# Kernel tuning notes

Measured on AMD Instinct MI355X. Metric: run time of the kernel, lower is better.

## Reference

```python
import jax, jax.numpy as jnp
import numpy as np

NEG_INF_DIAG = 1000000.0

def setup_inputs() -> dict:
    key = jax.random.key(0)
    k1, k2, k3 = jax.random.split(key, 3)
    B, N, S, D = 64, 32, 256, 128
    return {
        "query_embeddings": jax.random.normal(k1, (B, N, D), dtype=jnp.float32),
        "doc_embeddings": jax.random.normal(k2, (B, S, D), dtype=jnp.float32),
        "neg_doc_embeddings": jax.random.normal(k3, (B, S, D), dtype=jnp.float32),
    }

def _maxsim(q, d):
    # q: (b, n, dim), d: (b, s, dim) -> (b,) sum over n of max over s of q.d
    return jnp.einsum('bnd,bsd->bns', q, d).max(axis=2).sum(axis=1)

def reference(query_embeddings, doc_embeddings, neg_doc_embeddings):
    pos_scores = _maxsim(query_embeddings, doc_embeddings)
    neg_scores = _maxsim(query_embeddings, neg_doc_embeddings)
    loss = jax.nn.softplus(neg_scores - pos_scores).mean()

    # in-batch term: scores[b, c] = MaxSim(query b, doc c)
    scores = jnp.einsum('bnd,csd->bcns', query_embeddings, doc_embeddings).max(axis=3).sum(axis=2)  # (B, B)
    pos = jnp.diagonal(scores)
    B = scores.shape[0]
    neg = (scores - jnp.eye(B, dtype=scores.dtype) * NEG_INF_DIAG).max(axis=1)
    loss = loss + jax.nn.softplus(neg - pos).mean()
    return loss / 2
```

## Files before the change

kernel.cpp:

```cpp
#include <hip/hip_runtime.h>
#include <hip/hip_bf16.h>

#define B_SZ 64

typedef __attribute__((ext_vector_type(8))) short bf16x8;
typedef __attribute__((ext_vector_type(4))) float f32x4;

static __device__ __forceinline__ unsigned short f2bf(float f) {
    __hip_bfloat16 h = __float2bfloat16(f);
    return *reinterpret_cast<unsigned short*>(&h);
}

static __device__ __forceinline__ bf16x8 cvt_frag(const float* __restrict__ src) {
    float4 a = reinterpret_cast<const float4*>(src)[0];
    float4 b = reinterpret_cast<const float4*>(src)[1];
    union { bf16x8 v; unsigned short u[8]; } t;
    t.u[0] = f2bf(a.x); t.u[1] = f2bf(a.y); t.u[2] = f2bf(a.z); t.u[3] = f2bf(a.w);
    t.u[4] = f2bf(b.x); t.u[5] = f2bf(b.y); t.u[6] = f2bf(b.z); t.u[7] = f2bf(b.w);
    return t.v;
}

#define MFMA(A, Bv, C) __builtin_amdgcn_mfma_f32_16x16x32_bf16(A, Bv, C, 0, 0, 0)

__global__ __launch_bounds__(256, 2) void maxsim_mega(const float* __restrict__ q,
                                                      const float* __restrict__ dd,
                                                      const float* __restrict__ nd,
                                                      float* __restrict__ scores) {
    const int wg  = blockIdx.x;
    const int tid = threadIdx.x;
    const int wave = tid >> 6, lane = tid & 63;
    const int l15 = lane & 15, lhi = lane >> 4;

    __shared__ bf16x8 docL[4096];
    __shared__ bf16x8 qL[512];
    __shared__ float wred[8][4][4][8];

    int c, b0, nb;
    const float* docp;
    if (wg < 512) {
        const int x = wg & 7, i = wg >> 3;
        c   = x * 8 + (i & 7);
        b0  = (i >> 3) * 8;
        nb  = 8;
        docp = dd + (size_t)c * 32768;
    } else {
        b0 = wg - 512; c = 64; nb = 1;
        docp = nd + (size_t)b0 * 32768;
    }

    char* lb = reinterpret_cast<char*>(docL);
    #pragma unroll
    for (int i = 0; i < 16; ++i) {
        const int rem_g = i * 256 + tid;
        bf16x8 v = cvt_frag(docp + (size_t)rem_g * 8);
        const int ch = rem_g >> 10, rem = rem_g & 1023;
        const int a = ch * 16384 + ((rem * 16) ^ (((rem >> 4) & 7) << 4));
        *reinterpret_cast<bf16x8*>(lb + a) = v;
    }
    __syncthreads();

    bf16x8 Bv[4][4];
    #pragma unroll
    for (int kk = 0; kk < 4; ++kk)
        #pragma unroll
        for (int nt = 0; nt < 4; ++nt) {
            const int rem = (nt * 16 + l15) * 16 + kk * 4 + lhi;
            const int a = wave * 16384 + ((rem * 16) ^ (((rem >> 4) & 7) << 4));
            Bv[kk][nt] = *reinterpret_cast<const bf16x8*>(lb + a);
        }

    for (int bi = 0; bi < nb; ++bi) {
        const int b = b0 + bi;
        #pragma unroll
        for (int h = 0; h < 2; ++h) {
            const int g  = h * 256 + tid;
            const int n  = ((g >> 6) & 1) * 16 + (g & 15);
            const int k8 = (g >> 7) * 4 + ((g >> 4) & 3);
            qL[g] = cvt_frag(q + (size_t)b * 4096 + (size_t)(n * 16 + k8) * 8);
        }
        __syncthreads();

        bf16x8 Af[4][2];
        #pragma unroll
        for (int kk = 0; kk < 4; ++kk) {
            Af[kk][0] = qL[kk * 128 + lane];
            Af[kk][1] = qL[kk * 128 + 64 + lane];
        }
        f32x4 acc[2][4] = {};
        #pragma unroll
        for (int kk = 0; kk < 4; ++kk)
            #pragma unroll
            for (int nt = 0; nt < 4; ++nt) {
                acc[0][nt] = MFMA(Af[kk][0], Bv[kk][nt], acc[0][nt]);
                acc[1][nt] = MFMA(Af[kk][1], Bv[kk][nt], acc[1][nt]);
            }
        #pragma unroll
        for (int mt = 0; mt < 2; ++mt)
            #pragma unroll
            for (int r = 0; r < 4; ++r) {
                float m = fmaxf(fmaxf(acc[mt][0][r], acc[mt][1][r]),
                                fmaxf(acc[mt][2][r], acc[mt][3][r]));
                m = fmaxf(m, __shfl_xor(m, 1, 64));
                m = fmaxf(m, __shfl_xor(m, 2, 64));
                m = fmaxf(m, __shfl_xor(m, 4, 64));
                m = fmaxf(m, __shfl_xor(m, 8, 64));
                if (l15 == 0) wred[bi][wave][lhi][mt * 4 + r] = m;
            }
        __syncthreads();
    }

    if (tid < nb * 32) {
        const int bi = tid >> 5, n = tid & 31;
        const int slot = (n >> 4) * 4 + (n & 3);
        const int lh   = (n >> 2) & 3;
        float m = fmaxf(fmaxf(wred[bi][0][lh][slot], wred[bi][1][lh][slot]),
                        fmaxf(wred[bi][2][lh][slot], wred[bi][3][lh][slot]));
        m += __shfl_xor(m, 1, 32);
        m += __shfl_xor(m, 2, 32);
        m += __shfl_xor(m, 4, 32);
        m += __shfl_xor(m, 8, 32);
        m += __shfl_xor(m, 16, 32);
        if (n == 0) scores[(size_t)(b0 + bi) * 65 + c] = m;
    }
}

static __device__ __forceinline__ float softplusf(float x) {
    return fmaxf(x, 0.0f) + log1pf(expf(-fabsf(x)));
}

__global__ __launch_bounds__(64) void loss_kernel(const float* __restrict__ scores,
                                                  float* __restrict__ out) {
    const int b = threadIdx.x;
    const float* row = scores + b * 65;
    const float pos  = row[b];
    const float negq = row[64];
    float nib = -1e30f;
    #pragma unroll
    for (int c = 0; c < B_SZ; ++c) {
        float v = row[c] - ((c == b) ? 1000000.0f : 0.0f);
        nib = fmaxf(nib, v);
    }
    float t = softplusf(negq - pos) + softplusf(nib - pos);
    t += __shfl_xor(t, 1, 64);
    t += __shfl_xor(t, 2, 64);
    t += __shfl_xor(t, 4, 64);
    t += __shfl_xor(t, 8, 64);
    t += __shfl_xor(t, 16, 64);
    t += __shfl_xor(t, 32, 64);
    if (b == 0) out[0] = t * (0.5f / 64.0f);
}

extern "C" void kernel_launch(void* const* d_in, const int* in_sizes, int n_in,
                              void* d_out, int out_size, void* d_ws, size_t ws_size,
                              hipStream_t stream) {
    const float* q  = (const float*)d_in[0];
    const float* dd = (const float*)d_in[1];
    const float* nd = (const float*)d_in[2];
    float* out = (float*)d_out;

    float* scores = (float*)d_ws;

    maxsim_mega<<<512 + B_SZ, 256, 0, stream>>>(q, dd, nd, scores);
    loss_kernel<<<1, 64, 0, stream>>>(scores, out);
}
```

Before: 96.73 us.

## Load MFMA fragments directly from global memory, dropping LDS staging

Result: slower. 119.5 us (+23.6%).

```diff
diff --git a/kernel.cpp b/kernel.cpp
--- a/kernel.cpp
+++ b/kernel.cpp
@@ -22,17 +22,15 @@
 
 #define MFMA(A, Bv, C) __builtin_amdgcn_mfma_f32_16x16x32_bf16(A, Bv, C, 0, 0, 0)
 
-__global__ __launch_bounds__(256, 2) void maxsim_mega(const float* __restrict__ q,
-                                                      const float* __restrict__ dd,
-                                                      const float* __restrict__ nd,
-                                                      float* __restrict__ scores) {
+__global__ __launch_bounds__(256, 3) void maxsim_direct(const float* __restrict__ q,
+                                                        const float* __restrict__ dd,
+                                                        const float* __restrict__ nd,
+                                                        float* __restrict__ scores) {
     const int wg  = blockIdx.x;
     const int tid = threadIdx.x;
     const int wave = tid >> 6, lane = tid & 63;
     const int l15 = lane & 15, lhi = lane >> 4;
 
-    __shared__ bf16x8 docL[4096];
-    __shared__ bf16x8 qL[512];
     __shared__ float wred[8][4][4][8];
 
     int c, b0, nb;
@@ -48,43 +46,24 @@
         docp = nd + (size_t)b0 * 32768;
     }
 
-    char* lb = reinterpret_cast<char*>(docL);
-    #pragma unroll
-    for (int i = 0; i < 16; ++i) {
-        const int rem_g = i * 256 + tid;
-        bf16x8 v = cvt_frag(docp + (size_t)rem_g * 8);
-        const int ch = rem_g >> 10, rem = rem_g & 1023;
-        const int a = ch * 16384 + ((rem * 16) ^ (((rem >> 4) & 7) << 4));
-        *reinterpret_cast<bf16x8*>(lb + a) = v;
+    bf16x8 Bv[4][4];
+    {
+        const float* base = docp + (size_t)(wave * 64 + l15) * 128 + lhi * 8;
+        #pragma unroll
+        for (int kk = 0; kk < 4; ++kk)
+            #pragma unroll
+            for (int nt = 0; nt < 4; ++nt)
+                Bv[kk][nt] = cvt_frag(base + nt * 16 * 128 + kk * 32);
     }
-    __syncthreads();
 
-    bf16x8 Bv[4][4];
-    #pragma unroll
-    for (int kk = 0; kk < 4; ++kk)
-        #pragma unroll
-        for (int nt = 0; nt < 4; ++nt) {
-            const int rem = (nt * 16 + l15) * 16 + kk * 4 + lhi;
-            const int a = wave * 16384 + ((rem * 16) ^ (((rem >> 4) & 7) << 4));
-            Bv[kk][nt] = *reinterpret_cast<const bf16x8*>(lb + a);
-        }
-
+    const float* qbase = q + (size_t)b0 * 4096 + (size_t)l15 * 128 + lhi * 8;
     for (int bi = 0; bi < nb; ++bi) {
-        const int b = b0 + bi;
-        #pragma unroll
-        for (int h = 0; h < 2; ++h) {
-            const int g  = h * 256 + tid;
-            const int n  = ((g >> 6) & 1) * 16 + (g & 15);
-            const int k8 = (g >> 7) * 4 + ((g >> 4) & 3);
-            qL[g] = cvt_frag(q + (size_t)b * 4096 + (size_t)(n * 16 + k8) * 8);
-        }
-        __syncthreads();
-
         bf16x8 Af[4][2];
+        const float* qb = qbase + (size_t)bi * 4096;
         #pragma unroll
         for (int kk = 0; kk < 4; ++kk) {
-            Af[kk][0] = qL[kk * 128 + lane];
-            Af[kk][1] = qL[kk * 128 + 64 + lane];
+            Af[kk][0] = cvt_frag(qb + kk * 32);
+            Af[kk][1] = cvt_frag(qb + 16 * 128 + kk * 32);
         }
         f32x4 acc[2][4] = {};
         #pragma unroll
@@ -106,8 +85,8 @@
                 m = fmaxf(m, __shfl_xor(m, 8, 64));
                 if (l15 == 0) wred[bi][wave][lhi][mt * 4 + r] = m;
             }
-        __syncthreads();
     }
+    __syncthreads();
 
     if (tid < nb * 32) {
         const int bi = tid >> 5, n = tid & 31;
@@ -160,6 +139,6 @@
 
     float* scores = (float*)d_ws;
 
-    maxsim_mega<<<512 + B_SZ, 256, 0, stream>>>(q, dd, nd, scores);
+    maxsim_direct<<<512 + B_SZ, 256, 0, stream>>>(q, dd, nd, scores);
     loss_kernel<<<1, 64, 0, stream>>>(scores, out);
 }
```
